# Kernel optimization log

Measured on AMD Instinct MI355X. Metric: run time of the kernel, lower is better.

## Reference

```python
import jax, jax.numpy as jnp
import numpy as np

SEQ = 2048
D = 2048          # d_model
H = 16            # n_heads
DH = D // H       # dim_per_head = 128 (= pe_rotary_dims, full-head RoPE)
DFF = 4 * D
BACKGROUND_LEN = 1024
STYLE_VECS_LEN = 64


def setup_inputs() -> dict:
    key = jax.random.key(0)
    ks = jax.random.split(key, 12)
    s = 0.02
    f32 = jnp.float32
    return {
        "x": jax.random.normal(ks[0], (SEQ, D), f32),
        "attn_bias": jnp.zeros((SEQ, SEQ), f32),
        "ln_scale": jnp.ones((D,), f32),
        "ln_offset": jnp.zeros((D,), f32),
        "Wq": (jax.random.normal(ks[1], (D, D), f32) * s),
        "Wk": (jax.random.normal(ks[2], (D, D), f32) * s),
        "Wv": (jax.random.normal(ks[3], (D, D), f32) * s),
        "Wo": (jax.random.normal(ks[4], (D, D), f32) * s),
        "W1": (jax.random.normal(ks[5], (D, DFF), f32) * s),
        "b1": jnp.zeros((DFF,), f32),
        "W2": (jax.random.normal(ks[6], (DFF, D), f32) * s),
        "b2": jnp.zeros((D,), f32),
    }


def _layernorm(x, scale, offset):
    mean = jnp.mean(x, axis=-1, keepdims=True)
    var = jnp.var(x, axis=-1, keepdims=True)
    return scale * jax.lax.rsqrt(var + 1e-5) * (x - mean) + offset


def _rotate_every_two(x):
    # x: (T, H, d) -> interleaved (-x2, x1)
    x1 = x[:, :, ::2]
    x2 = x[:, :, 1::2]
    return jnp.stack((-x2, x1), axis=-1).reshape(x.shape)


def _apply_rope(q, k):
    rd = q.shape[-1]
    inv_freq = 1.0 / 10000 ** (np.arange(0, rd, 2) / rd)  # (rd/2,)
    pos = jnp.arange(k.shape[0])
    sinusoid = pos[:, None] * inv_freq[None, :]           # (T, rd/2)
    # repeat 'b n -> b (n j)', j=2  ==  elementwise repeat along last axis
    sin = jnp.repeat(jnp.sin(sinusoid), 2, axis=-1)[:, None, :]  # (T,1,rd)
    cos = jnp.repeat(jnp.cos(sinusoid), 2, axis=-1)[:, None, :]
    q = q * cos + _rotate_every_two(q) * sin
    k = k * cos + _rotate_every_two(k) * sin
    return q, k


def _causal_bottleneck_bias():
    mask = np.tril(np.ones((SEQ, SEQ), np.float32))
    # DO_CAUSAL_BOTTLENECK: tokens after background+style cannot see background
    mask[BACKGROUND_LEN + STYLE_VECS_LEN:, :BACKGROUND_LEN] = 0.0
    return jnp.asarray(-1e10 * (1.0 - mask))


def reference(x, attn_bias, ln_scale, ln_offset, Wq, Wk, Wv, Wo, W1, b1, W2, b2):
    # f_psum / g_psum are identities with cores_per_replica == 1
    xn = _layernorm(x, ln_scale, ln_offset)                      # (T, D)

    q = (xn @ Wq).reshape(SEQ, H, DH)
    k = (xn @ Wk).reshape(SEQ, H, DH)
    v = (xn @ Wv).reshape(SEQ, H, DH)

    q, k = _apply_rope(q, k)  # pe_rotary_dims == dim_per_head: rotate whole head

    logits = jnp.einsum('thd,Thd->htT', q, k) / np.sqrt(DH).astype(x.dtype)
    bias = _causal_bottleneck_bias() + attn_bias                 # (T, T)
    logits = logits + bias[None, :, :]
    weights = jax.nn.softmax(logits, axis=-1)                    # (H, T, T)

    attn_vec = jnp.einsum('htT,Thd->thd', weights, v).reshape(SEQ, D)
    attn_out = attn_vec @ Wo                                     # (T, D)

    ff = jax.nn.gelu(xn @ W1 + b1) @ W2 + b2                     # (T, D)
    return attn_out + ff
```

## Files before the change

### kernel.cpp

```cpp
#include <hip/hip_runtime.h>

#define SEQ 2048
#define DMODEL 2048
#define NH 16
#define DH 128
#define DFF 8192

typedef __bf16 bf16x8 __attribute__((ext_vector_type(8)));
typedef float f32x4 __attribute__((ext_vector_type(4)));
typedef int i32x4 __attribute__((ext_vector_type(4)));

__device__ __forceinline__ float b2f(unsigned short u) {
    union { float f; unsigned int i; } v; v.i = ((unsigned int)u) << 16; return v.f;
}
__device__ __forceinline__ unsigned short f2b(float f) {
    union { float f; unsigned int i; } v; v.f = f;
    unsigned int i = v.i;
    i += 0x7fffu + ((i >> 16) & 1u);
    return (unsigned short)(i >> 16);
}
__device__ __forceinline__ bf16x8 ldfrag(const unsigned short* p) {
    return *(const bf16x8*)p;
}
__device__ __forceinline__ void async_ld16(const unsigned short* g, unsigned short* l) {
    __builtin_amdgcn_global_load_lds(
        (const __attribute__((address_space(1))) unsigned int*)g,
        (__attribute__((address_space(3))) unsigned int*)l, 16, 0, 0);
}
__device__ __forceinline__ float loadef(const void* p, long i, int isf) {
    return isf ? ((const float*)p)[i] : b2f(((const unsigned short*)p)[i]);
}
__device__ __forceinline__ void load8f(const void* p, long i, int isf, float* v) {
    if (isf) {
        i32x4 r0 = *(const i32x4*)((const float*)p + i);
        i32x4 r1 = *(const i32x4*)((const float*)p + i + 4);
        const float* f0 = (const float*)&r0;
        const float* f1 = (const float*)&r1;
#pragma unroll
        for (int j = 0; j < 4; j++) { v[j] = f0[j]; v[4 + j] = f1[j]; }
    } else {
        i32x4 raw = *(const i32x4*)((const unsigned short*)p + i);
        const unsigned short* u = (const unsigned short*)&raw;
#pragma unroll
        for (int j = 0; j < 8; j++) v[j] = b2f(u[j]);
    }
}

__global__ __launch_bounds__(256) void detect_kernel(const unsigned short* __restrict__ x,
                                                     int* __restrict__ flag)
{
    const int tid = threadIdx.x;
    int bad = 0;
#pragma unroll
    for (int i = 0; i < 16; i++) {
        unsigned short u = x[tid * 16 + i];
        int e = (u >> 7) & 0xFF;
        if (e >= 0x90) bad = 1;
    }
    unsigned long long b = __ballot(bad);
    __shared__ int r[4];
    if ((tid & 63) == 0) r[tid >> 6] = (b != 0ull);
    __syncthreads();
    if (tid == 0) *flag = (r[0] | r[1] | r[2] | r[3]) ? 1 : 0;
}

__global__ __launch_bounds__(256) void ln_kernel(
    const void* __restrict__ x,
    const void* __restrict__ sc,
    const void* __restrict__ of,
    unsigned short* __restrict__ xn,
    const int* __restrict__ fl)
{
    const int isf = *fl;
    const int row = blockIdx.x, tid = threadIdx.x;
    float v[8]; float s = 0.f, sq = 0.f;
    load8f(x, (long)row * DMODEL + tid * 8, isf, v);
#pragma unroll
    for (int i = 0; i < 8; i++) { s += v[i]; sq += v[i] * v[i]; }
#pragma unroll
    for (int off = 1; off < 64; off <<= 1) { s += __shfl_xor(s, off); sq += __shfl_xor(sq, off); }
    __shared__ float red[8];
    const int w = tid >> 6, l = tid & 63;
    if (l == 0) { red[w * 2] = s; red[w * 2 + 1] = sq; }
    __syncthreads();
    s  = red[0] + red[2] + red[4] + red[6];
    sq = red[1] + red[3] + red[5] + red[7];
    const float mean = s * (1.0f / DMODEL);
    const float var  = sq * (1.0f / DMODEL) - mean * mean;
    const float rsig = rsqrtf(var + 1e-5f);
    __align__(16) unsigned short o[8];
#pragma unroll
    for (int i = 0; i < 8; i++) {
        int c = tid * 8 + i;
        o[i] = f2b(loadef(sc, c, isf) * (v[i] - mean) * rsig + loadef(of, c, isf));
    }
    *(i32x4*)(xn + (long)row * DMODEL + tid * 8) = *(const i32x4*)o;
}

__global__ __launch_bounds__(1024) void transpose_w(
    const void* __restrict__ in0, const void* __restrict__ in1,
    const void* __restrict__ in2, const void* __restrict__ in3,
    unsigned short* __restrict__ out, int R, int C,
    const int* __restrict__ fl)
{
    const int isf = *fl;
    const int z = blockIdx.z;
    const void* in = (z == 0) ? in0 : (z == 1) ? in1 : (z == 2) ? in2 : in3;
    unsigned short* dst = out + (long)z * R * C;
    __shared__ unsigned int tile[32][33];
    const int tx = threadIdx.x, ty = threadIdx.y;
    const int c0 = blockIdx.x * 32, r0 = blockIdx.y * 64;
    const float a0 = loadef(in, (long)(r0 + 2 * ty)     * C + c0 + tx, isf);
    const float a1 = loadef(in, (long)(r0 + 2 * ty + 1) * C + c0 + tx, isf);
    tile[ty][tx] = (unsigned)f2b(a0) | ((unsigned)f2b(a1) << 16);
    __syncthreads();
    *(unsigned int*)(dst + (long)(c0 + ty) * R + r0 + 2 * tx) = tile[tx][ty];
}

__global__ __launch_bounds__(256) void rope_kernel(unsigned short* q, unsigned short* k)
{
    const int idx = blockIdx.x * 256 + threadIdx.x;
    const int i = idx & 63;
    const int h = (idx >> 6) & 15;
    const int t = idx >> 10;
    const long base = (long)t * DMODEL + h * DH + 2 * i;
    const float inv = __expf(-(float)i * (9.210340371976184f / 64.0f));
    float sn, cs;
    sincosf((float)t * inv, &sn, &cs);
    {
        float a = b2f(q[base]), b = b2f(q[base + 1]);
        q[base]     = f2b(a * cs - b * sn);
        q[base + 1] = f2b(b * cs + a * sn);
    }
    {
        float a = b2f(k[base]), b = b2f(k[base + 1]);
        k[base]     = f2b(a * cs - b * sn);
        k[base + 1] = f2b(b * cs + a * sn);
    }
}

template<int EPI>
__global__ __launch_bounds__(256) void gemm_bt(
    const unsigned short* __restrict__ A,
    const unsigned short* __restrict__ Bt,
    const void* __restrict__ bias,
    const unsigned short* __restrict__ add,
    void* __restrict__ Cout,
    int M, int N, int K, int Ks,
    const int* __restrict__ fl)
{
    const int isf = fl ? *fl : 0;
    __shared__ __align__(16) unsigned short lA[128 * 64];
    __shared__ __align__(16) unsigned short lB[128 * 64];
    const int tid = threadIdx.x;
    const int l = tid & 63, w = tid >> 6;
    const int quad = l >> 4, lq = l & 15;
    const long bm = (long)blockIdx.y * 128, bn = (long)blockIdx.x * 128;
    const int wm = (w >> 1) * 64, wn = (w & 1) * 64;
    const int kofs = (EPI == 5) ? blockIdx.z * Ks : 0;

    const int r8 = l >> 3;
    const int csw = ((l & 7) ^ r8) * 8;
    const unsigned short* Ag = A  + (bm + w * 32 + r8) * (long)K + kofs + csw;
    const unsigned short* Bg = Bt + (bn + w * 32 + r8) * (long)K + kofs + csw;
    unsigned short* lAd = lA + w * 2048 + l * 8;
    unsigned short* lBd = lB + w * 2048 + l * 8;
    const long K8 = 8 * (long)K;

    f32x4 acc[4][4] = {};

    for (int k0 = 0; k0 < Ks; k0 += 64) {
#pragma unroll
        for (int q = 0; q < 4; q++) {
            async_ld16(Ag + k0 + q * K8, lAd + q * 512);
            async_ld16(Bg + k0 + q * K8, lBd + q * 512);
        }
        __syncthreads();
#pragma unroll
        for (int hk = 0; hk < 2; hk++) {
            bf16x8 af[4], bfv[4];
#pragma unroll
            for (int i = 0; i < 4; i++) {
                const int row = wm + i * 16 + lq;
                af[i] = ldfrag(lA + row * 64 + ((hk * 4 + quad) ^ (lq & 7)) * 8);
            }
#pragma unroll
            for (int j = 0; j < 4; j++) {
                const int row = wn + j * 16 + lq;
                bfv[j] = ldfrag(lB + row * 64 + ((hk * 4 + quad) ^ (lq & 7)) * 8);
            }
#pragma unroll
            for (int i = 0; i < 4; i++)
#pragma unroll
                for (int j = 0; j < 4; j++)
                    acc[i][j] = __builtin_amdgcn_mfma_f32_16x16x32_bf16(af[i], bfv[j], acc[i][j], 0, 0, 0);
        }
        __syncthreads();
    }

#pragma unroll
    for (int i = 0; i < 4; i++)
#pragma unroll
        for (int j = 0; j < 4; j++)
#pragma unroll
            for (int r = 0; r < 4; r++) {
                const long t = bm + wm + i * 16 + quad * 4 + r;
                const long n = bn + wn + j * 16 + lq;
                float v = acc[i][j][r];
                if constexpr (EPI == 5) {
                    ((float*)Cout)[(long)blockIdx.z * M * N + t * N + n] = v;
                } else if constexpr (EPI == 4) {
                    unsigned short* base = (unsigned short*)Cout;
                    if (n < 4096)
                        base[(n >> 11) * (long)(SEQ * DMODEL) + t * DMODEL + (n & 2047)] = f2b(v);
                    else {
                        const long np = n - 4096;
                        base[2L * SEQ * DMODEL + (np >> 7) * (long)(DH * SEQ) + (np & 127) * (long)SEQ + t] = f2b(v);
                    }
                } else if constexpr (EPI == 3) {
                    v += loadef(bias, n, isf) + b2f(add[t * (long)N + n]);
                    if (isf) ((float*)Cout)[t * (long)N + n] = v;
                    else     ((unsigned short*)Cout)[t * (long)N + n] = f2b(v);
                } else {
                    if constexpr (EPI == 2) {
                        v += loadef(bias, n, isf);
                        const float u = 0.7978845608028654f * (v + 0.044715f * v * v * v);
                        v = v * (1.0f - __builtin_amdgcn_rcpf(1.0f + __expf(2.0f * u)));
                    }
                    ((unsigned short*)Cout)[t * (long)N + n] = f2b(v);
                }
            }
}

__global__ __launch_bounds__(256) void reduce_out(
    const float* __restrict__ P, int nsplit,
    const unsigned short* __restrict__ aout,
    const void* __restrict__ b2,
    void* __restrict__ out,
    const int* __restrict__ fl)
{
    const int isf = *fl;
    const long i = ((long)blockIdx.x * 256 + threadIdx.x) * 4;
    f32x4 s = *(const f32x4*)(P + i);
    for (int z = 1; z < nsplit; z++) s += *(const f32x4*)(P + (long)z * SEQ * DMODEL + i);
    const unsigned short* a4 = aout + i;
    float v[4];
#pragma unroll
    for (int c = 0; c < 4; c++)
        v[c] = s[c] + b2f(a4[c]) + loadef(b2, (i + c) & (DMODEL - 1), isf);
    if (isf) {
        f32x4 o; o[0] = v[0]; o[1] = v[1]; o[2] = v[2]; o[3] = v[3];
        *(f32x4*)((float*)out + i) = o;
    } else {
        __align__(8) unsigned short o[4];
#pragma unroll
        for (int c = 0; c < 4; c++) o[c] = f2b(v[c]);
        *(unsigned long long*)((unsigned short*)out + i) = *(const unsigned long long*)o;
    }
}

__global__ __launch_bounds__(256) void flash_attn(
    const unsigned short* __restrict__ q,
    const unsigned short* __restrict__ k,
    const unsigned short* __restrict__ vT,
    const void* __restrict__ bias,
    unsigned short* __restrict__ outp,
    const int* __restrict__ fl)
{
    const int isf = *fl;
    __shared__ __align__(16) unsigned short lK[64 * 136];
    __shared__ __align__(16) unsigned short lV[128 * 72];
    __shared__ __align__(16) unsigned short lP[4 * 16 * 72];
    const int tid = threadIdx.x;
    const int l = tid & 63, w = tid >> 6;
    const int quad = l >> 4, lq = l & 15;
    const int qb = blockIdx.x * 64;
    const int h = blockIdx.y;

    bf16x8 aq[4];
#pragma unroll
    for (int c = 0; c < 4; c++)
        aq[c] = ldfrag(q + (long)(qb + 16 * w + lq) * DMODEL + h * DH + 32 * c + quad * 8);

    f32x4 accO[8] = {};
    float m_i[4], l_i[4];
#pragma unroll
    for (int r = 0; r < 4; r++) { m_i[r] = -1e30f; l_i[r] = 0.f; }

    const int Tstart = (qb >= 1088) ? 1024 : 0;
    unsigned short* lPw = lP + w * (16 * 72);

    for (int Tt = Tstart; Tt < qb + 64; Tt += 64) {
        __syncthreads();
#pragma unroll
        for (int s = 0; s < 4; s++) {
            const int cc = tid + 256 * s;
            const int rr = cc >> 4, d0 = (cc & 15) * 8;
            *(i32x4*)(lK + rr * 136 + d0) =
                *(const i32x4*)(k + (long)(Tt + rr) * DMODEL + h * DH + d0);
            const int dd = cc >> 3, t0 = (cc & 7) * 8;
            *(i32x4*)(lV + dd * 72 + t0) =
                *(const i32x4*)(vT + (long)h * (DH * SEQ) + (long)dd * SEQ + Tt + t0);
        }
        __syncthreads();

        float sv[4][4];
        float mx[4] = { -1e30f, -1e30f, -1e30f, -1e30f };
#pragma unroll
        for (int j = 0; j < 4; j++) {
            f32x4 accS = {};
#pragma unroll
            for (int c = 0; c < 4; c++) {
                bf16x8 bk = ldfrag(lK + (j * 16 + lq) * 136 + 32 * c + quad * 8);
                accS = __builtin_amdgcn_mfma_f32_16x16x32_bf16(aq[c], bk, accS, 0, 0, 0);
            }
            const int Tcol = Tt + j * 16 + lq;
#pragma unroll
            for (int r = 0; r < 4; r++) {
                const int trow = qb + 16 * w + quad * 4 + r;
                float s;
                if (Tcol > trow) s = -1e30f;
                else s = accS[r] * 0.08838834764831845f + loadef(bias, (long)trow * SEQ + Tcol, isf);
                sv[j][r] = s;
                mx[r] = fmaxf(mx[r], s);
            }
        }
#pragma unroll
        for (int r = 0; r < 4; r++) {
            mx[r] = fmaxf(mx[r], __shfl_xor(mx[r], 1));
            mx[r] = fmaxf(mx[r], __shfl_xor(mx[r], 2));
            mx[r] = fmaxf(mx[r], __shfl_xor(mx[r], 4));
            mx[r] = fmaxf(mx[r], __shfl_xor(mx[r], 8));
        }
        float alpha[4];
#pragma unroll
        for (int r = 0; r < 4; r++) {
            const float mn = fmaxf(m_i[r], mx[r]);
            alpha[r] = __expf(m_i[r] - mn);
            m_i[r] = mn;
            float sum = 0.f;
#pragma unroll
            for (int j = 0; j < 4; j++) {
                const float p = __expf(sv[j][r] - mn);
                sv[j][r] = p;
                sum += p;
            }
            sum += __shfl_xor(sum, 1);
            sum += __shfl_xor(sum, 2);
            sum += __shfl_xor(sum, 4);
            sum += __shfl_xor(sum, 8);
            l_i[r] = l_i[r] * alpha[r] + sum;
        }
#pragma unroll
        for (int j = 0; j < 4; j++)
#pragma unroll
            for (int r = 0; r < 4; r++)
                lPw[(quad * 4 + r) * 72 + j * 16 + lq] = f2b(sv[j][r]);
#pragma unroll
        for (int jd = 0; jd < 8; jd++)
#pragma unroll
            for (int r = 0; r < 4; r++)
                accO[jd][r] *= alpha[r];
        const bf16x8 ap0 = ldfrag(lPw + lq * 72 + quad * 8);
        const bf16x8 ap1 = ldfrag(lPw + lq * 72 + 32 + quad * 8);
#pragma unroll
        for (int jd = 0; jd < 8; jd++) {
            bf16x8 bv0 = ldfrag(lV + (jd * 16 + lq) * 72 + quad * 8);
            accO[jd] = __builtin_amdgcn_mfma_f32_16x16x32_bf16(ap0, bv0, accO[jd], 0, 0, 0);
            bf16x8 bv1 = ldfrag(lV + (jd * 16 + lq) * 72 + 32 + quad * 8);
            accO[jd] = __builtin_amdgcn_mfma_f32_16x16x32_bf16(ap1, bv1, accO[jd], 0, 0, 0);
        }
    }
#pragma unroll
    for (int r = 0; r < 4; r++) {
        const float inv = 1.0f / l_i[r];
        const long trow = qb + 16 * w + quad * 4 + r;
#pragma unroll
        for (int jd = 0; jd < 8; jd++)
            outp[trow * (long)DMODEL + h * DH + jd * 16 + lq] = f2b(accO[jd][r] * inv);
    }
}

extern "C" void kernel_launch(void* const* d_in, const int* in_sizes, int n_in,
                              void* d_out, int out_size, void* d_ws, size_t ws_size,
                              hipStream_t stream)
{
    (void)in_sizes; (void)n_in; (void)out_size;
    const void* x         = d_in[0];
    const void* attn_bias = d_in[1];
    const void* ln_scale  = d_in[2];
    const void* ln_offset = d_in[3];
    const void* Wq = d_in[4];
    const void* Wk = d_in[5];
    const void* Wv = d_in[6];
    const void* Wo = d_in[7];
    const void* W1 = d_in[8];
    const void* b1 = d_in[9];
    const void* W2 = d_in[10];
    const void* b2 = d_in[11];

    char* ws = (char*)d_ws;
    unsigned short* wT   = (unsigned short*)(ws);
    unsigned short* xn   = (unsigned short*)(ws + (32ull << 20));
    unsigned short* qv   = (unsigned short*)(ws + (40ull << 20));
    unsigned short* kv   = (unsigned short*)(ws + (48ull << 20));
    unsigned short* vTb  = (unsigned short*)(ws + (56ull << 20));
    unsigned short* avec = (unsigned short*)(ws + (64ull << 20));
    unsigned short* aout = (unsigned short*)(ws + (72ull << 20));
    unsigned short* hff  = (unsigned short*)(ws + (40ull << 20));
    int* flag            = (int*)(ws + (80ull << 20));
    float* Pf            = (float*)(ws + (81ull << 20));

    (void)vTb; (void)kv;

    int nsplit = 1;
    if (ws_size >= (145ull << 20)) nsplit = 4;
    else if (ws_size >= (113ull << 20)) nsplit = 2;

    const dim3 tb(32, 32);

    detect_kernel<<<1, 256, 0, stream>>>((const unsigned short*)x, flag);

    ln_kernel<<<SEQ, 256, 0, stream>>>(x, ln_scale, ln_offset, xn, flag);

    transpose_w<<<dim3(64, 32, 4), tb, 0, stream>>>(Wq, Wk, Wv, Wo, wT, DMODEL, DMODEL, flag);

    gemm_bt<4><<<dim3(48, 16), 256, 0, stream>>>(xn, wT, nullptr, nullptr, qv,
                                                 SEQ, 3 * DMODEL, DMODEL, DMODEL, flag);

    rope_kernel<<<(SEQ * NH * DH / 2) / 256, 256, 0, stream>>>(qv, kv);

    flash_attn<<<dim3(SEQ / 64, NH), 256, 0, stream>>>(qv, kv, vTb, attn_bias, avec, flag);

    gemm_bt<0><<<dim3(16, 16), 256, 0, stream>>>(avec, wT + 12ull * 1024 * 1024, nullptr, nullptr, aout,
                                                 SEQ, DMODEL, DMODEL, DMODEL, flag);

    transpose_w<<<dim3(DFF / 32, DMODEL / 64), tb, 0, stream>>>(W1, W1, W1, W1, wT, DMODEL, DFF, flag);
    gemm_bt<2><<<dim3(DFF / 128, SEQ / 128), 256, 0, stream>>>(xn, wT, b1, nullptr, hff,
                                                               SEQ, DFF, DMODEL, DMODEL, flag);

    transpose_w<<<dim3(DMODEL / 32, DFF / 64), tb, 0, stream>>>(W2, W2, W2, W2, wT, DFF, DMODEL, flag);
    if (nsplit > 1) {
        gemm_bt<5><<<dim3(16, 16, nsplit), 256, 0, stream>>>(hff, wT, nullptr, nullptr, Pf,
                                                             SEQ, DMODEL, DFF, DFF / nsplit, flag);
        reduce_out<<<(SEQ * DMODEL) / (256 * 4), 256, 0, stream>>>(Pf, nsplit, aout, b2, d_out, flag);
    } else {
        gemm_bt<3><<<dim3(16, 16), 256, 0, stream>>>(hff, wT, b2, aout, d_out,
                                                     SEQ, DMODEL, DFF, DFF, flag);
    }
}
```

Baseline: 699.6 us.

## Stage K, V and bias tiles into LDS via async loads with XOR swizzle

Flash attention now stages its K, V and bias tiles into shared memory with direct global-to-LDS async loads instead of register round-trips. Bank conflicts are avoided with an XOR swizzle on the tile columns rather than row padding. The bias tile is loaded once per block, replacing per-element scattered global reads in the score loop. Waves whose rows are fully masked for a tile now skip its compute, at the cost of extra LDS use and more complex indexing.

```diff
diff --git a/kernel.cpp b/kernel.cpp
--- a/kernel.cpp
+++ b/kernel.cpp
@@ -22,7 +22,7 @@
 __device__ __forceinline__ bf16x8 ldfrag(const unsigned short* p) {
     return *(const bf16x8*)p;
 }
-__device__ __forceinline__ void async_ld16(const unsigned short* g, unsigned short* l) {
+__device__ __forceinline__ void async_ld16(const void* g, void* l) {
     __builtin_amdgcn_global_load_lds(
         (const __attribute__((address_space(1))) unsigned int*)g,
         (__attribute__((address_space(3))) unsigned int*)l, 16, 0, 0);
@@ -268,9 +268,11 @@
     const int* __restrict__ fl)
 {
     const int isf = *fl;
-    __shared__ __align__(16) unsigned short lK[64 * 136];
-    __shared__ __align__(16) unsigned short lV[128 * 72];
+    __shared__ __align__(16) unsigned short lK[64 * 128];
+    __shared__ __align__(16) unsigned short lV[128 * 64];
+    __shared__ __align__(16) float          lBf[64 * 64];
     __shared__ __align__(16) unsigned short lP[4 * 16 * 72];
+    unsigned short* lBh = (unsigned short*)lBf;
     const int tid = threadIdx.x;
     const int l = tid & 63, w = tid >> 6;
     const int quad = l >> 4, lq = l & 15;
@@ -289,20 +291,46 @@
 
     const int Tstart = (qb >= 1088) ? 1024 : 0;
     unsigned short* lPw = lP + w * (16 * 72);
+    const int rowmax_w = qb + 16 * w + 15;
+
+    const unsigned short* kh = k + h * DH;
+    const unsigned short* vh = vT + (long)h * (DH * SEQ);
 
     for (int Tt = Tstart; Tt < qb + 64; Tt += 64) {
         __syncthreads();
 #pragma unroll
         for (int s = 0; s < 4; s++) {
-            const int cc = tid + 256 * s;
-            const int rr = cc >> 4, d0 = (cc & 15) * 8;
-            *(i32x4*)(lK + rr * 136 + d0) =
-                *(const i32x4*)(k + (long)(Tt + rr) * DMODEL + h * DH + d0);
-            const int dd = cc >> 3, t0 = (cc & 7) * 8;
-            *(i32x4*)(lV + dd * 72 + t0) =
-                *(const i32x4*)(vT + (long)h * (DH * SEQ) + (long)dd * SEQ + Tt + t0);
+            const int ci = s * 256 + tid;
+            const int rr = ci >> 4, p = ci & 15;
+            async_ld16(kh + (long)(Tt + rr) * DMODEL + (p ^ (rr & 15)) * 8,
+                       lK + ci * 8);
+        }
+#pragma unroll
+        for (int s = 0; s < 4; s++) {
+            const int ci = s * 256 + tid;
+            const int dd = ci >> 3, p = ci & 7;
+            async_ld16(vh + (long)dd * SEQ + Tt + (p ^ (dd & 7)) * 8,
+                       lV + ci * 8);
+        }
+        if (isf) {
+            const float* bsrc = (const float*)bias;
+#pragma unroll
+            for (int s = 0; s < 4; s++) {
+                const int ci = s * 256 + tid;
+                const int rr = ci >> 4, cc = ci & 15;
+                async_ld16(bsrc + (long)(qb + rr) * SEQ + Tt + cc * 4, lBf + ci * 4);
+            }
+        } else {
+            const unsigned short* bsrc = (const unsigned short*)bias;
+#pragma unroll
+            for (int s = 0; s < 2; s++) {
+                const int ci = s * 256 + tid;
+                const int rr = ci >> 3, cc = ci & 7;
+                async_ld16(bsrc + (long)(qb + rr) * SEQ + Tt + cc * 8, lBh + ci * 8);
+            }
         }
         __syncthreads();
+        if (Tt > rowmax_w) continue;
 
         float sv[4][4];
         float mx[4] = { -1e30f, -1e30f, -1e30f, -1e30f };
@@ -311,16 +339,21 @@
             f32x4 accS = {};
 #pragma unroll
             for (int c = 0; c < 4; c++) {
-                bf16x8 bk = ldfrag(lK + (j * 16 + lq) * 136 + 32 * c + quad * 8);
+                bf16x8 bk = ldfrag(lK + (j * 16 + lq) * 128 + ((4 * c + quad) ^ lq) * 8);
                 accS = __builtin_amdgcn_mfma_f32_16x16x32_bf16(aq[c], bk, accS, 0, 0, 0);
             }
             const int Tcol = Tt + j * 16 + lq;
 #pragma unroll
             for (int r = 0; r < 4; r++) {
-                const int trow = qb + 16 * w + quad * 4 + r;
+                const int rloc = 16 * w + quad * 4 + r;
+                const int trow = qb + rloc;
                 float s;
                 if (Tcol > trow) s = -1e30f;
-                else s = accS[r] * 0.08838834764831845f + loadef(bias, (long)trow * SEQ + Tcol, isf);
+                else {
+                    const float bv = isf ? lBf[rloc * 64 + j * 16 + lq]
+                                         : b2f(lBh[rloc * 64 + j * 16 + lq]);
+                    s = accS[r] * 0.08838834764831845f + bv;
+                }
                 sv[j][r] = s;
                 mx[r] = fmaxf(mx[r], s);
             }
@@ -365,9 +398,9 @@
         const bf16x8 ap1 = ldfrag(lPw + lq * 72 + 32 + quad * 8);
 #pragma unroll
         for (int jd = 0; jd < 8; jd++) {
-            bf16x8 bv0 = ldfrag(lV + (jd * 16 + lq) * 72 + quad * 8);
+            bf16x8 bv0 = ldfrag(lV + (jd * 16 + lq) * 64 + (quad ^ (lq & 7)) * 8);
             accO[jd] = __builtin_amdgcn_mfma_f32_16x16x32_bf16(ap0, bv0, accO[jd], 0, 0, 0);
-            bf16x8 bv1 = ldfrag(lV + (jd * 16 + lq) * 72 + 32 + quad * 8);
+            bf16x8 bv1 = ldfrag(lV + (jd * 16 + lq) * 64 + ((quad + 4) ^ (lq & 7)) * 8);
             accO[jd] = __builtin_amdgcn_mfma_f32_16x16x32_bf16(ap1, bv1, accO[jd], 0, 0, 0);
         }
     }
@@ -411,8 +444,6 @@
     int* flag            = (int*)(ws + (80ull << 20));
     float* Pf            = (float*)(ws + (81ull << 20));
 
-    (void)vTb; (void)kv;
-
     int nsplit = 1;
     if (ws_size >= (145ull << 20)) nsplit = 4;
     else if (ws_size >= (113ull << 20)) nsplit = 2;
```

Measured after the change: 644.9 us. 7.8% less time.
